# Kernel optimization log

Measured on AMD Instinct MI355X. Metric: run time of the kernel, lower is better.

Reference implementation:

```python
import jax, jax.numpy as jnp
import numpy as np
import math

HIDDEN_DIM = 1024
N_HEAD = 16
HEAD_DIM = HIDDEN_DIM // N_HEAD
BS, SEQ = 2, 4096


def setup_inputs() -> dict:
    key = jax.random.key(0)
    ks = jax.random.split(key, 6)
    s = 1.0 / math.sqrt(HIDDEN_DIM)
    return {
        "x": jax.random.normal(ks[0], (BS, SEQ, HIDDEN_DIM), dtype=jnp.float32),
        "attention_mask": jnp.zeros((1, 1, SEQ, SEQ), dtype=jnp.float32),
        "wq_w": jax.random.normal(ks[1], (HIDDEN_DIM, HIDDEN_DIM), dtype=jnp.float32) * s,
        "wq_b": jnp.zeros((HIDDEN_DIM,), dtype=jnp.float32),
        "wk_w": jax.random.normal(ks[2], (HIDDEN_DIM, HIDDEN_DIM), dtype=jnp.float32) * s,
        "wk_b": jnp.zeros((HIDDEN_DIM,), dtype=jnp.float32),
        "wv_w": jax.random.normal(ks[3], (HIDDEN_DIM, HIDDEN_DIM), dtype=jnp.float32) * s,
        "wv_b": jnp.zeros((HIDDEN_DIM,), dtype=jnp.float32),
        "wo_w": jax.random.normal(ks[4], (HIDDEN_DIM, HIDDEN_DIM), dtype=jnp.float32) * s,
        "wo_b": jnp.zeros((HIDDEN_DIM,), dtype=jnp.float32),
    }


def reference(x, attention_mask, wq_w, wq_b, wk_w, wk_b, wv_w, wv_b, wo_w, wo_b):
    bs, seq_len, _ = x.shape
    # nn.Linear: y = x @ W.T + b
    Q = x @ wq_w.T + wq_b
    K = x @ wk_w.T + wk_b
    V = x @ wv_w.T + wv_b
    # [bs, n_head, seq, head_dim]
    Q = Q.reshape(bs, seq_len, N_HEAD, HEAD_DIM).transpose(0, 2, 1, 3)
    K = K.reshape(bs, seq_len, N_HEAD, HEAD_DIM).transpose(0, 2, 1, 3)
    V = V.reshape(bs, seq_len, N_HEAD, HEAD_DIM).transpose(0, 2, 1, 3)
    scale = 1.0 / math.sqrt(HEAD_DIM)
    att = jnp.einsum('bhqd,bhkd->bhqk', Q, K) * scale
    att = att + attention_mask
    att = jax.nn.softmax(att, axis=-1)
    # dropout is identity in eval mode (p=0.1 during training)
    out = jnp.einsum('bhqk,bhkd->bhqd', att, V)
    out = out.transpose(0, 2, 1, 3).reshape(bs, seq_len, HIDDEN_DIM)
    return out @ wo_w.T + wo_b
```

## Files before the change

### kernel.cpp

```cpp
#include <hip/hip_runtime.h>

typedef unsigned short u16;
typedef __bf16 bf16x4 __attribute__((ext_vector_type(4)));
typedef __bf16 bf16x8 __attribute__((ext_vector_type(8)));
typedef float f32x4 __attribute__((ext_vector_type(4)));

#define SEQ_LEN 4096
#define HID 1024
#define NHEAD 16
#define HDIM 64
#define MROWS 8192
#define LOG2E 1.44269504088896f

__device__ __forceinline__ u16 f2bf(float f) {
  union { float f; unsigned u; } v; v.f = f;
  unsigned r = v.u + 0x7fffu + ((v.u >> 16) & 1u);
  return (u16)(r >> 16);
}

__device__ __forceinline__ float fexp2(float x) {
  float r;
  asm("v_exp_f32 %0, %1" : "=v"(r) : "v"(x));
  return r;
}

__device__ __forceinline__ void gload16(const void* g, void* lds) {
  __builtin_amdgcn_global_load_lds((const __attribute__((address_space(1))) void*)g,
                                   (__attribute__((address_space(3))) void*)lds, 16, 0, 0);
}


__global__ void prep_kernel(const float* __restrict__ x,
                            const float* __restrict__ w0, const float* __restrict__ w1,
                            const float* __restrict__ w2, const float* __restrict__ w3,
                            const float* __restrict__ mask,
                            u16* __restrict__ xb, u16* __restrict__ wb, int* __restrict__ flag) {
  const int NX = MROWS * HID / 4;
  const int NW = HID * HID / 4;
  const int NM = SEQ_LEN * SEQ_LEN / 4;
  const int TOT = NX + 4 * NW + NM;
  int stride = gridDim.x * blockDim.x;
  bool nz = false;
  for (int i = blockIdx.x * blockDim.x + threadIdx.x; i < TOT; i += stride) {
    if (i < NX) {
      float4 v = ((const float4*)x)[i];
      ((ushort4*)xb)[i] = make_ushort4(f2bf(v.x), f2bf(v.y), f2bf(v.z), f2bf(v.w));
    } else if (i < NX + 4 * NW) {
      int j = i - NX;
      int mat = j >> 18;
      int off = j & (NW - 1);
      const float* src = (mat == 0) ? w0 : (mat == 1) ? w1 : (mat == 2) ? w2 : w3;
      float4 v = ((const float4*)src)[off];
      ((ushort4*)(wb + (size_t)mat * HID * HID))[off] =
          make_ushort4(f2bf(v.x), f2bf(v.y), f2bf(v.z), f2bf(v.w));
    } else {
      int j = i - NX - 4 * NW;
      float4 v = ((const float4*)mask)[j];
      nz |= (v.x != 0.f) | (v.y != 0.f) | (v.z != 0.f) | (v.w != 0.f);
    }
  }
  if (__any(nz) && (threadIdx.x & 63) == 0) atomicOr(flag, 1);
}


__device__ __forceinline__ void gemm_core(const u16* __restrict__ A, const u16* __restrict__ W,
                                          int m0, int n0, char* As, char* Bs, f32x4 acc[4][4]) {
  const int t = threadIdx.x, w = t >> 6, l = t & 63;
  const int lr = l & 15, lg = l >> 4;
  const int wr = (w >> 1) * 64, wc = (w & 1) * 64;
#pragma unroll
  for (int i = 0; i < 4; i++)
#pragma unroll
    for (int j = 0; j < 4; j++) acc[i][j] = (f32x4){0.f, 0.f, 0.f, 0.f};

  for (int k0 = 0; k0 < HID; k0 += 64) {
    __syncthreads();
#pragma unroll
    for (int j = 0; j < 4; j++) {
      int o = w * 4096 + j * 1024 + l * 16;
      int row = o >> 7, kb = (o >> 4) & 7, skb = kb ^ (row & 7);
      gload16(A + (size_t)(m0 + row) * HID + k0 + skb * 8, As + (w * 4096 + j * 1024));
      gload16(W + (size_t)(n0 + row) * HID + k0 + skb * 8, Bs + (w * 4096 + j * 1024));
    }
    __syncthreads();
#pragma unroll
    for (int ks = 0; ks < 2; ks++) {
      bf16x8 af[4], bf[4];
      int kb = ks * 4 + lg;
#pragma unroll
      for (int mt = 0; mt < 4; mt++) {
        int row = wr + mt * 16 + lr;
        af[mt] = *(const bf16x8*)(As + row * 128 + ((kb ^ (row & 7)) << 4));
      }
#pragma unroll
      for (int nt = 0; nt < 4; nt++) {
        int row = wc + nt * 16 + lr;
        bf[nt] = *(const bf16x8*)(Bs + row * 128 + ((kb ^ (row & 7)) << 4));
      }
#pragma unroll
      for (int mt = 0; mt < 4; mt++)
#pragma unroll
        for (int nt = 0; nt < 4; nt++)
          acc[mt][nt] = __builtin_amdgcn_mfma_f32_16x16x32_bf16(af[mt], bf[nt], acc[mt][nt], 0, 0, 0);
    }
  }
}

__global__ __launch_bounds__(256) void gemm_qkv_kernel(
    const u16* __restrict__ xb, const u16* __restrict__ wqb, const u16* __restrict__ wkb,
    const u16* __restrict__ wvb, const float* __restrict__ bq, const float* __restrict__ bk,
    const float* __restrict__ bv, u16* __restrict__ Qb, u16* __restrict__ Kb, u16* __restrict__ VT) {
  __shared__ __align__(128) char lds[32768];
  int flat = blockIdx.y * 64 + blockIdx.x;
  int xcd = flat & 7, j = flat >> 3;
  int bx = xcd * 8 + (j & 7);
  int by = j >> 3;
  int m0 = bx * 128;
  int ng = by * 128;
  int mat = ng >> 10, n0 = ng & 1023;
  const u16* W = (mat == 0) ? wqb : (mat == 1) ? wkb : wvb;
  const float* bias = (mat == 0) ? bq : (mat == 1) ? bk : bv;
  f32x4 acc[4][4];
  gemm_core(xb, W, m0, n0, lds, lds + 16384, acc);

  const int t = threadIdx.x, w = t >> 6, l = t & 63;
  const int lr = l & 15, lg = l >> 4;
  if (mat < 2) {
    u16* dst = (mat == 0) ? Qb : Kb;
    float scale = (mat == 0) ? 0.125f * LOG2E : 1.0f;
#pragma unroll
    for (int mt = 0; mt < 4; mt++)
#pragma unroll
      for (int nt = 0; nt < 4; nt++) {
        int n = n0 + (w & 1) * 64 + nt * 16 + lr;
        float bn = bias[n];
#pragma unroll
        for (int i = 0; i < 4; i++) {
          int m = m0 + (w >> 1) * 64 + mt * 16 + lg * 4 + i;
          dst[(size_t)m * HID + n] = f2bf((acc[mt][nt][i] + bn) * scale);
        }
      }
  } else {
#pragma unroll
    for (int mt = 0; mt < 4; mt++)
#pragma unroll
      for (int nt = 0; nt < 4; nt++) {
        int m = m0 + (w >> 1) * 64 + mt * 16 + lg * 4;
        int n = n0 + (w & 1) * 64 + nt * 16 + lr;
        int b = m >> 12, s = m & 4095;
        int h = n >> 6, d = n & 63;
        int t4 = (s >> 2) & 15;
        int t4p = ((t4 & 8)) | ((t4 & 3) << 1) | ((t4 >> 2) & 1);
        int sp = (s & ~63) | (t4p << 2);
        float bn = bias[n];
        ushort4 pk = make_ushort4(f2bf(acc[mt][nt][0] + bn), f2bf(acc[mt][nt][1] + bn),
                                  f2bf(acc[mt][nt][2] + bn), f2bf(acc[mt][nt][3] + bn));
        *(ushort4*)(VT + (((size_t)(b * NHEAD + h) * HDIM + d) * SEQ_LEN + sp)) = pk;
      }
  }
}

__global__ __launch_bounds__(256) void gemm_out_kernel(
    const u16* __restrict__ Ob, const u16* __restrict__ wob, const float* __restrict__ bo,
    float* __restrict__ out) {
  __shared__ __align__(128) char lds[32768];
  int flat = blockIdx.y * 64 + blockIdx.x;
  int xcd = flat & 7, j = flat >> 3;
  int bx = xcd * 8 + (j & 7);
  int by = j >> 3;
  int m0 = bx * 128, n0 = by * 128;
  f32x4 acc[4][4];
  gemm_core(Ob, wob, m0, n0, lds, lds + 16384, acc);
  const int t = threadIdx.x, w = t >> 6, l = t & 63;
  const int lr = l & 15, lg = l >> 4;
#pragma unroll
  for (int mt = 0; mt < 4; mt++)
#pragma unroll
    for (int nt = 0; nt < 4; nt++) {
      int n = n0 + (w & 1) * 64 + nt * 16 + lr;
      float bn = bo[n];
#pragma unroll
      for (int i = 0; i < 4; i++) {
        int m = m0 + (w >> 1) * 64 + mt * 16 + lg * 4 + i;
        out[(size_t)m * HID + n] = acc[mt][nt][i] + bn;
      }
    }
}

__global__ __launch_bounds__(256, 2) void attn_kernel(
    const u16* __restrict__ Qb, const u16* __restrict__ Kb, const u16* __restrict__ VT,
    const float* __restrict__ mask, const int* __restrict__ flag, u16* __restrict__ Ob) {
  __shared__ __align__(128) char lds[32768];
  const int flat = blockIdx.x;
  const int xcd = flat & 7;
  const int slot = flat >> 3;
  const int bh = xcd * 4 + (slot >> 5);
  const int bx = slot & 31;
  const int q0 = bx * 128;
  const int b = bh >> 4, h = bh & 15;
  const int t = threadIdx.x, w = t >> 6, l = t & 63;
  const int lr = l & 15, lg = l >> 4;
  const bool useMask = (flag[0] != 0);
  int qrow[2];
#pragma unroll
  for (int s = 0; s < 2; s++) qrow[s] = q0 + (w * 2 + s) * 16 + lr;

  bf16x8 qf[2][2];
#pragma unroll
  for (int s = 0; s < 2; s++) {
    const u16* qp = Qb + (size_t)(b * SEQ_LEN + qrow[s]) * HID + h * HDIM;
#pragma unroll
    for (int ks = 0; ks < 2; ks++) qf[s][ks] = *(const bf16x8*)(qp + (ks * 4 + lg) * 8);
  }

  bf16x8 ones;
#pragma unroll
  for (int j = 0; j < 8; j++) ones[j] = (__bf16)1.0f;

  f32x4 oacc[2][4];
#pragma unroll
  for (int s = 0; s < 2; s++)
#pragma unroll
    for (int dt = 0; dt < 4; dt++) oacc[s][dt] = (f32x4){0.f, 0.f, 0.f, 0.f};
  f32x4 lacc[2] = {(f32x4){0.f, 0.f, 0.f, 0.f}, (f32x4){0.f, 0.f, 0.f, 0.f}};
  float m_r[2] = {-1e30f, -1e30f};

  int off[2][4];
#pragma unroll
  for (int ks = 0; ks < 2; ks++) {
    int kb = ks * 4 + lg;
#pragma unroll
    for (int kt = 0; kt < 4; kt++) {
      int row = kt * 16 + lr;
      off[ks][kt] = row * 128 + ((kb ^ (row & 7)) << 4);
    }
  }

  const int o0 = t * 16;
  const int o1 = o0 + 4096;
  const int r0 = t >> 3;
  const int r1 = r0 + 32;
  const int sk0 = (t & 7) ^ (r0 & 7);
  const int sk1 = (t & 7) ^ (r1 & 7);
  const u16* kg0 = Kb + (size_t)(b * SEQ_LEN) * HID + h * HDIM + (size_t)r0 * HID + sk0 * 8;
  const u16* kg1 = Kb + (size_t)(b * SEQ_LEN) * HID + h * HDIM + (size_t)r1 * HID + sk1 * 8;
  const u16* vg0 = VT + ((size_t)(b * NHEAD + h) * HDIM + r0) * SEQ_LEN + sk0 * 8;
  const u16* vg1 = VT + ((size_t)(b * NHEAD + h) * HDIM + r1) * SEQ_LEN + sk1 * 8;

#define STAGE(BI)                                            \
  do {                                                       \
    gload16(kg0, lds + (BI) * 8192 + o0);                    \
    gload16(kg1, lds + (BI) * 8192 + o1);                    \
    gload16(vg0, lds + 16384 + (BI) * 8192 + o0);            \
    gload16(vg1, lds + 16384 + (BI) * 8192 + o1);            \
    kg0 += 64 * HID; kg1 += 64 * HID; vg0 += 64; vg1 += 64;  \
  } while (0)

#define QKPART(BI)                                                                         \
    const char* Ks = lds + (BI) * 8192;                                                    \
    const char* Vs = lds + 16384 + (BI) * 8192;                                            \
    bf16x8 kf[2][4];                                                                       \
    _Pragma("unroll") for (int ks = 0; ks < 2; ks++)                                       \
    _Pragma("unroll") for (int kt = 0; kt < 4; kt++)                                       \
        kf[ks][kt] = *(const bf16x8*)(Ks + off[ks][kt]);                                   \
    f32x4 sf[2][4];                                                                        \
    _Pragma("unroll") for (int s = 0; s < 2; s++)                                          \
    _Pragma("unroll") for (int kt = 0; kt < 4; kt++) sf[s][kt] = (f32x4){0.f,0.f,0.f,0.f}; \
    __builtin_amdgcn_s_setprio(1);                                                         \
    _Pragma("unroll") for (int ks = 0; ks < 2; ks++)                                       \
    _Pragma("unroll") for (int s = 0; s < 2; s++)                                          \
    _Pragma("unroll") for (int kt = 0; kt < 4; kt++)                                       \
        sf[s][kt] = __builtin_amdgcn_mfma_f32_16x16x32_bf16(kf[ks][kt], qf[s][ks],         \
                                                            sf[s][kt], 0, 0, 0);          \
    __builtin_amdgcn_s_setprio(0);

#define PVPART                                                                             \
    bf16x8 vf[2][4];                                                                       \
    _Pragma("unroll") for (int ks = 0; ks < 2; ks++)                                       \
    _Pragma("unroll") for (int dt = 0; dt < 4; dt++)                                       \
        vf[ks][dt] = *(const bf16x8*)(Vs + off[ks][dt]);                                   \
    __builtin_amdgcn_s_setprio(1);                                                         \
    _Pragma("unroll") for (int s = 0; s < 2; s++) {                                        \
      _Pragma("unroll") for (int ks = 0; ks < 2; ks++) {                                   \
        bf16x8 pb;                                                                         \
        _Pragma("unroll") for (int j = 0; j < 4; j++) pb[j] = (__bf16)sf[s][2 * ks][j];    \
        _Pragma("unroll") for (int j = 0; j < 4; j++) pb[4 + j] = (__bf16)sf[s][2*ks+1][j];\
        _Pragma("unroll") for (int dt = 0; dt < 4; dt++)                                   \
            oacc[s][dt] =                                                                  \
                __builtin_amdgcn_mfma_f32_16x16x32_bf16(vf[ks][dt], pb, oacc[s][dt],0,0,0);\
        lacc[s] = __builtin_amdgcn_mfma_f32_16x16x32_bf16(ones, pb, lacc[s], 0, 0, 0);     \
      }                                                                                    \
    }                                                                                      \
    __builtin_amdgcn_s_setprio(0);

#define COMPUTE_FAST(BI)                                                                   \
  do {                                                                                     \
    QKPART(BI)                                                                             \
    _Pragma("unroll") for (int s = 0; s < 2; s++)                                          \
    _Pragma("unroll") for (int kt = 0; kt < 4; kt++)                                       \
    _Pragma("unroll") for (int i = 0; i < 4; i++)                                          \
        sf[s][kt][i] = fexp2(sf[s][kt][i]);                                                \
    PVPART                                                                                 \
  } while (0)

#define COMPUTE_SAFE(BI, KV0)                                                              \
  do {                                                                                     \
    QKPART(BI)                                                                             \
    _Pragma("unroll") for (int s = 0; s < 2; s++)                                          \
    _Pragma("unroll") for (int kt = 0; kt < 4; kt++)                                       \
    _Pragma("unroll") for (int i = 0; i < 4; i++)                                          \
        sf[s][kt][i] +=                                                                    \
            mask[(size_t)qrow[s] * SEQ_LEN + (KV0) + kt * 16 + lg * 4 + i] * LOG2E;        \
    float mx[2];                                                                           \
    _Pragma("unroll") for (int s = 0; s < 2; s++) {                                        \
      float m1 = fmaxf(fmaxf(sf[s][0][0], sf[s][0][1]), sf[s][0][2]);                      \
      m1 = fmaxf(fmaxf(m1, sf[s][0][3]), sf[s][1][0]);                                     \
      m1 = fmaxf(fmaxf(m1, sf[s][1][1]), sf[s][1][2]);                                     \
      m1 = fmaxf(fmaxf(m1, sf[s][1][3]), sf[s][2][0]);                                     \
      m1 = fmaxf(fmaxf(m1, sf[s][2][1]), sf[s][2][2]);                                     \
      m1 = fmaxf(fmaxf(m1, sf[s][2][3]), sf[s][3][0]);                                     \
      m1 = fmaxf(fmaxf(m1, sf[s][3][1]), sf[s][3][2]);                                     \
      m1 = fmaxf(m1, sf[s][3][3]);                                                         \
      m1 = fmaxf(m1, __shfl_xor(m1, 16));                                                  \
      mx[s] = fmaxf(m1, __shfl_xor(m1, 32));                                               \
    }                                                                                      \
    if (__any(fmaxf(mx[0] - m_r[0], mx[1] - m_r[1]) > 8.0f)) {                             \
      _Pragma("unroll") for (int s = 0; s < 2; s++) {                                      \
        float nm = fmaxf(m_r[s], mx[s]);                                                   \
        float scf = fexp2(m_r[s] - nm);                                                    \
        m_r[s] = nm;                                                                       \
        _Pragma("unroll") for (int dt = 0; dt < 4; dt++)                                   \
        _Pragma("unroll") for (int i = 0; i < 4; i++) oacc[s][dt][i] *= scf;               \
        lacc[s] *= scf;                                                                    \
      }                                                                                    \
    }                                                                                      \
    _Pragma("unroll") for (int s = 0; s < 2; s++)                                          \
    _Pragma("unroll") for (int kt = 0; kt < 4; kt++)                                       \
    _Pragma("unroll") for (int i = 0; i < 4; i++)                                          \
        sf[s][kt][i] = fexp2(sf[s][kt][i] - m_r[s]);                                       \
    PVPART                                                                                 \
  } while (0)

  STAGE(0);
  __syncthreads();

  const int NT = SEQ_LEN / 64;
  if (!useMask) {
    for (int t2 = 0; t2 < NT / 2; ++t2) {
      STAGE(1);
      COMPUTE_FAST(0);
      __syncthreads();
      if (t2 != NT / 2 - 1) STAGE(0);
      COMPUTE_FAST(1);
      __syncthreads();
    }
  } else {
    for (int t2 = 0; t2 < NT / 2; ++t2) {
      STAGE(1);
      COMPUTE_SAFE(0, t2 * 128);
      __syncthreads();
      if (t2 != NT / 2 - 1) STAGE(0);
      COMPUTE_SAFE(1, t2 * 128 + 64);
      __syncthreads();
    }
  }
#undef STAGE
#undef QKPART
#undef PVPART
#undef COMPUTE_FAST
#undef COMPUTE_SAFE

#pragma unroll
  for (int s = 0; s < 2; s++) {
    float inv = 1.0f / lacc[s][0];
    u16* orow = Ob + (size_t)(b * SEQ_LEN + qrow[s]) * HID + h * HDIM;
#pragma unroll
    for (int dt = 0; dt < 4; dt++) {
      ushort4 pk = make_ushort4(f2bf(oacc[s][dt][0] * inv), f2bf(oacc[s][dt][1] * inv),
                                f2bf(oacc[s][dt][2] * inv), f2bf(oacc[s][dt][3] * inv));
      *(ushort4*)(orow + dt * 16 + lg * 4) = pk;
    }
  }
}


extern "C" void kernel_launch(void* const* d_in, const int* in_sizes, int n_in,
                              void* d_out, int out_size, void* d_ws, size_t ws_size,
                              hipStream_t stream) {
  const float* x    = (const float*)d_in[0];
  const float* mask = (const float*)d_in[1];
  const float* wq   = (const float*)d_in[2];
  const float* bq   = (const float*)d_in[3];
  const float* wk   = (const float*)d_in[4];
  const float* bk   = (const float*)d_in[5];
  const float* wv   = (const float*)d_in[6];
  const float* bv   = (const float*)d_in[7];
  const float* wo   = (const float*)d_in[8];
  const float* bo   = (const float*)d_in[9];

  char* ws = (char*)d_ws;
  u16* xb  = (u16*)(ws + 0);
  u16* wqb = (u16*)(ws + 16777216);
  u16* Qb  = (u16*)(ws + 25165824);
  u16* Kb  = (u16*)(ws + 41943040);
  u16* VT  = (u16*)(ws + 58720256);
  int* flag = (int*)(ws + 75497472);
  u16* wkb = wqb + 1048576;
  u16* wvb = wqb + 2097152;
  u16* wob = wqb + 3145728;
  u16* Ob = xb;

  (void)hipMemsetAsync(flag, 0, 4, stream);
  prep_kernel<<<2048, 256, 0, stream>>>(x, wq, wk, wv, wo, mask, xb, wqb, flag);
  gemm_qkv_kernel<<<dim3(64, 24), 256, 0, stream>>>(xb, wqb, wkb, wvb, bq, bk, bv, Qb, Kb, VT);
  attn_kernel<<<1024, 256, 0, stream>>>(Qb, Kb, VT, mask, flag, Ob);
  gemm_out_kernel<<<dim3(64, 8), 256, 0, stream>>>(Ob, wob, bo, (float*)d_out);
}
```

Baseline: 245.4 us.

## Double query tile per attention block to 256 rows, split KV tile into halves

Each attention block now handles 256 query rows, with each wave owning 64 rows, so every staged K/V tile in shared memory is reused by twice as many queries. The grid drops from 1024 to 512 blocks, which halves global K/V traffic. Each 64-key tile is processed in two 32-key halves to limit register pressure from the doubled accumulators. The trade-offs are higher VGPR use, which may lower occupancy under launch_bounds(256,2), and fewer blocks to spread across CUs.

```diff
diff --git a/kernel.cpp b/kernel.cpp
--- a/kernel.cpp
+++ b/kernel.cpp
@@ -194,20 +194,20 @@
   const int flat = blockIdx.x;
   const int xcd = flat & 7;
   const int slot = flat >> 3;
-  const int bh = xcd * 4 + (slot >> 5);
-  const int bx = slot & 31;
-  const int q0 = bx * 128;
+  const int bh = xcd * 4 + (slot >> 4);
+  const int bx = slot & 15;
+  const int q0 = bx * 256;
   const int b = bh >> 4, h = bh & 15;
   const int t = threadIdx.x, w = t >> 6, l = t & 63;
   const int lr = l & 15, lg = l >> 4;
   const bool useMask = (flag[0] != 0);
-  int qrow[2];
-#pragma unroll
-  for (int s = 0; s < 2; s++) qrow[s] = q0 + (w * 2 + s) * 16 + lr;
-
-  bf16x8 qf[2][2];
-#pragma unroll
-  for (int s = 0; s < 2; s++) {
+  int qrow[4];
+#pragma unroll
+  for (int s = 0; s < 4; s++) qrow[s] = q0 + w * 64 + s * 16 + lr;
+
+  bf16x8 qf[4][2];
+#pragma unroll
+  for (int s = 0; s < 4; s++) {
     const u16* qp = Qb + (size_t)(b * SEQ_LEN + qrow[s]) * HID + h * HDIM;
 #pragma unroll
     for (int ks = 0; ks < 2; ks++) qf[s][ks] = *(const bf16x8*)(qp + (ks * 4 + lg) * 8);
@@ -217,13 +217,15 @@
 #pragma unroll
   for (int j = 0; j < 8; j++) ones[j] = (__bf16)1.0f;
 
-  f32x4 oacc[2][4];
-#pragma unroll
-  for (int s = 0; s < 2; s++)
+  f32x4 oacc[4][4];
+#pragma unroll
+  for (int s = 0; s < 4; s++)
 #pragma unroll
     for (int dt = 0; dt < 4; dt++) oacc[s][dt] = (f32x4){0.f, 0.f, 0.f, 0.f};
-  f32x4 lacc[2] = {(f32x4){0.f, 0.f, 0.f, 0.f}, (f32x4){0.f, 0.f, 0.f, 0.f}};
-  float m_r[2] = {-1e30f, -1e30f};
+  f32x4 lacc[4];
+#pragma unroll
+  for (int s = 0; s < 4; s++) lacc[s] = (f32x4){0.f, 0.f, 0.f, 0.f};
+  float m_r[4] = {-1e30f, -1e30f, -1e30f, -1e30f};
 
   int off[2][4];
 #pragma unroll
@@ -256,76 +258,75 @@
     kg0 += 64 * HID; kg1 += 64 * HID; vg0 += 64; vg1 += 64;  \
   } while (0)
 
-#define QKPART(BI)                                                                         \
+#define HALF_HEAD(Ks, H)                                                                   \
+    bf16x8 kf[2][2];                                                                       \
+    _Pragma("unroll") for (int ks = 0; ks < 2; ks++)                                       \
+    _Pragma("unroll") for (int ktl = 0; ktl < 2; ktl++)                                    \
+        kf[ks][ktl] = *(const bf16x8*)((Ks) + off[ks][2 * (H) + ktl]);                     \
+    f32x4 sf[4][2];                                                                        \
+    _Pragma("unroll") for (int s = 0; s < 4; s++)                                          \
+    _Pragma("unroll") for (int ktl = 0; ktl < 2; ktl++) sf[s][ktl] = (f32x4){0,0,0,0};     \
+    __builtin_amdgcn_s_setprio(1);                                                         \
+    _Pragma("unroll") for (int ks = 0; ks < 2; ks++)                                       \
+    _Pragma("unroll") for (int s = 0; s < 4; s++)                                          \
+    _Pragma("unroll") for (int ktl = 0; ktl < 2; ktl++)                                    \
+        sf[s][ktl] = __builtin_amdgcn_mfma_f32_16x16x32_bf16(kf[ks][ktl], qf[s][ks],       \
+                                                             sf[s][ktl], 0, 0, 0);        \
+    __builtin_amdgcn_s_setprio(0);
+
+#define HALF_TAIL(Vs, H)                                                                   \
+    bf16x8 vf[4];                                                                          \
+    _Pragma("unroll") for (int dt = 0; dt < 4; dt++)                                       \
+        vf[dt] = *(const bf16x8*)((Vs) + off[H][dt]);                                      \
+    bf16x8 pb[4];                                                                          \
+    _Pragma("unroll") for (int s = 0; s < 4; s++) {                                        \
+      _Pragma("unroll") for (int j = 0; j < 4; j++) pb[s][j] = (__bf16)sf[s][0][j];        \
+      _Pragma("unroll") for (int j = 0; j < 4; j++) pb[s][4 + j] = (__bf16)sf[s][1][j];    \
+    }                                                                                      \
+    __builtin_amdgcn_s_setprio(1);                                                         \
+    _Pragma("unroll") for (int s = 0; s < 4; s++) {                                        \
+      _Pragma("unroll") for (int dt = 0; dt < 4; dt++)                                     \
+          oacc[s][dt] =                                                                    \
+              __builtin_amdgcn_mfma_f32_16x16x32_bf16(vf[dt], pb[s], oacc[s][dt], 0,0,0);  \
+      lacc[s] = __builtin_amdgcn_mfma_f32_16x16x32_bf16(ones, pb[s], lacc[s], 0, 0, 0);    \
+    }                                                                                      \
+    __builtin_amdgcn_s_setprio(0);
+
+#define HALF_FAST(BI, H)                                                                   \
+  do {                                                                                     \
     const char* Ks = lds + (BI) * 8192;                                                    \
     const char* Vs = lds + 16384 + (BI) * 8192;                                            \
-    bf16x8 kf[2][4];                                                                       \
-    _Pragma("unroll") for (int ks = 0; ks < 2; ks++)                                       \
-    _Pragma("unroll") for (int kt = 0; kt < 4; kt++)                                       \
-        kf[ks][kt] = *(const bf16x8*)(Ks + off[ks][kt]);                                   \
-    f32x4 sf[2][4];                                                                        \
-    _Pragma("unroll") for (int s = 0; s < 2; s++)                                          \
-    _Pragma("unroll") for (int kt = 0; kt < 4; kt++) sf[s][kt] = (f32x4){0.f,0.f,0.f,0.f}; \
-    __builtin_amdgcn_s_setprio(1);                                                         \
-    _Pragma("unroll") for (int ks = 0; ks < 2; ks++)                                       \
-    _Pragma("unroll") for (int s = 0; s < 2; s++)                                          \
-    _Pragma("unroll") for (int kt = 0; kt < 4; kt++)                                       \
-        sf[s][kt] = __builtin_amdgcn_mfma_f32_16x16x32_bf16(kf[ks][kt], qf[s][ks],         \
-                                                            sf[s][kt], 0, 0, 0);          \
-    __builtin_amdgcn_s_setprio(0);
-
-#define PVPART                                                                             \
-    bf16x8 vf[2][4];                                                                       \
-    _Pragma("unroll") for (int ks = 0; ks < 2; ks++)                                       \
-    _Pragma("unroll") for (int dt = 0; dt < 4; dt++)                                       \
-        vf[ks][dt] = *(const bf16x8*)(Vs + off[ks][dt]);                                   \
-    __builtin_amdgcn_s_setprio(1);                                                         \
-    _Pragma("unroll") for (int s = 0; s < 2; s++) {                                        \
-      _Pragma("unroll") for (int ks = 0; ks < 2; ks++) {                                   \
-        bf16x8 pb;                                                                         \
-        _Pragma("unroll") for (int j = 0; j < 4; j++) pb[j] = (__bf16)sf[s][2 * ks][j];    \
-        _Pragma("unroll") for (int j = 0; j < 4; j++) pb[4 + j] = (__bf16)sf[s][2*ks+1][j];\
-        _Pragma("unroll") for (int dt = 0; dt < 4; dt++)                                   \
-            oacc[s][dt] =                                                                  \
-                __builtin_amdgcn_mfma_f32_16x16x32_bf16(vf[ks][dt], pb, oacc[s][dt],0,0,0);\
-        lacc[s] = __builtin_amdgcn_mfma_f32_16x16x32_bf16(ones, pb, lacc[s], 0, 0, 0);     \
-      }                                                                                    \
-    }                                                                                      \
-    __builtin_amdgcn_s_setprio(0);
-
-#define COMPUTE_FAST(BI)                                                                   \
+    HALF_HEAD(Ks, H)                                                                       \
+    _Pragma("unroll") for (int s = 0; s < 4; s++)                                          \
+    _Pragma("unroll") for (int ktl = 0; ktl < 2; ktl++)                                    \
+    _Pragma("unroll") for (int i = 0; i < 4; i++)                                          \
+        sf[s][ktl][i] = fexp2(sf[s][ktl][i]);                                              \
+    HALF_TAIL(Vs, H)                                                                       \
+  } while (0)
+
+#define HALF_SAFE(BI, H, KV0)                                                              \
   do {                                                                                     \
-    QKPART(BI)                                                                             \
-    _Pragma("unroll") for (int s = 0; s < 2; s++)                                          \
-    _Pragma("unroll") for (int kt = 0; kt < 4; kt++)                                       \
+    const char* Ks = lds + (BI) * 8192;                                                    \
+    const char* Vs = lds + 16384 + (BI) * 8192;                                            \
+    HALF_HEAD(Ks, H)                                                                       \
+    _Pragma("unroll") for (int s = 0; s < 4; s++)                                          \
+    _Pragma("unroll") for (int ktl = 0; ktl < 2; ktl++)                                    \
     _Pragma("unroll") for (int i = 0; i < 4; i++)                                          \
-        sf[s][kt][i] = fexp2(sf[s][kt][i]);                                                \
-    PVPART                                                                                 \
-  } while (0)
-
-#define COMPUTE_SAFE(BI, KV0)                                                              \
-  do {                                                                                     \
-    QKPART(BI)                                                                             \
-    _Pragma("unroll") for (int s = 0; s < 2; s++)                                          \
-    _Pragma("unroll") for (int kt = 0; kt < 4; kt++)                                       \
-    _Pragma("unroll") for (int i = 0; i < 4; i++)                                          \
-        sf[s][kt][i] +=                                                                    \
-            mask[(size_t)qrow[s] * SEQ_LEN + (KV0) + kt * 16 + lg * 4 + i] * LOG2E;        \
-    float mx[2];                                                                           \
-    _Pragma("unroll") for (int s = 0; s < 2; s++) {                                        \
+        sf[s][ktl][i] += mask[(size_t)qrow[s] * SEQ_LEN + (KV0) + (2 * (H) + ktl) * 16 +   \
+                              lg * 4 + i] * LOG2E;                                         \
+    float mx[4];                                                                           \
+    _Pragma("unroll") for (int s = 0; s < 4; s++) {                                        \
       float m1 = fmaxf(fmaxf(sf[s][0][0], sf[s][0][1]), sf[s][0][2]);                      \
       m1 = fmaxf(fmaxf(m1, sf[s][0][3]), sf[s][1][0]);                                     \
       m1 = fmaxf(fmaxf(m1, sf[s][1][1]), sf[s][1][2]);                                     \
-      m1 = fmaxf(fmaxf(m1, sf[s][1][3]), sf[s][2][0]);                                     \
-      m1 = fmaxf(fmaxf(m1, sf[s][2][1]), sf[s][2][2]);                                     \
-      m1 = fmaxf(fmaxf(m1, sf[s][2][3]), sf[s][3][0]);                                     \
-      m1 = fmaxf(fmaxf(m1, sf[s][3][1]), sf[s][3][2]);                                     \
-      m1 = fmaxf(m1, sf[s][3][3]);                                                         \
+      m1 = fmaxf(m1, sf[s][1][3]);                                                         \
       m1 = fmaxf(m1, __shfl_xor(m1, 16));                                                  \
       mx[s] = fmaxf(m1, __shfl_xor(m1, 32));                                               \
     }                                                                                      \
-    if (__any(fmaxf(mx[0] - m_r[0], mx[1] - m_r[1]) > 8.0f)) {                             \
-      _Pragma("unroll") for (int s = 0; s < 2; s++) {                                      \
+    float dmax = fmaxf(fmaxf(mx[0] - m_r[0], mx[1] - m_r[1]),                              \
+                       fmaxf(mx[2] - m_r[2], mx[3] - m_r[3]));                             \
+    if (__any(dmax > 8.0f)) {                                                              \
+      _Pragma("unroll") for (int s = 0; s < 4; s++) {                                      \
         float nm = fmaxf(m_r[s], mx[s]);                                                   \
         float scf = fexp2(m_r[s] - nm);                                                    \
         m_r[s] = nm;                                                                       \
@@ -334,11 +335,11 @@
         lacc[s] *= scf;                                                                    \
       }                                                                                    \
     }                                                                                      \
-    _Pragma("unroll") for (int s = 0; s < 2; s++)                                          \
-    _Pragma("unroll") for (int kt = 0; kt < 4; kt++)                                       \
+    _Pragma("unroll") for (int s = 0; s < 4; s++)                                          \
+    _Pragma("unroll") for (int ktl = 0; ktl < 2; ktl++)                                    \
     _Pragma("unroll") for (int i = 0; i < 4; i++)                                          \
-        sf[s][kt][i] = fexp2(sf[s][kt][i] - m_r[s]);                                       \
-    PVPART                                                                                 \
+        sf[s][ktl][i] = fexp2(sf[s][ktl][i] - m_r[s]);                                     \
+    HALF_TAIL(Vs, H)                                                                       \
   } while (0)
 
   STAGE(0);
@@ -348,30 +349,34 @@
   if (!useMask) {
     for (int t2 = 0; t2 < NT / 2; ++t2) {
       STAGE(1);
-      COMPUTE_FAST(0);
+      HALF_FAST(0, 0);
+      HALF_FAST(0, 1);
       __syncthreads();
       if (t2 != NT / 2 - 1) STAGE(0);
-      COMPUTE_FAST(1);
+      HALF_FAST(1, 0);
+      HALF_FAST(1, 1);
       __syncthreads();
     }
   } else {
     for (int t2 = 0; t2 < NT / 2; ++t2) {
       STAGE(1);
-      COMPUTE_SAFE(0, t2 * 128);
+      HALF_SAFE(0, 0, t2 * 128);
+      HALF_SAFE(0, 1, t2 * 128);
       __syncthreads();
       if (t2 != NT / 2 - 1) STAGE(0);
-      COMPUTE_SAFE(1, t2 * 128 + 64);
+      HALF_SAFE(1, 0, t2 * 128 + 64);
+      HALF_SAFE(1, 1, t2 * 128 + 64);
       __syncthreads();
     }
   }
 #undef STAGE
-#undef QKPART
-#undef PVPART
-#undef COMPUTE_FAST
-#undef COMPUTE_SAFE
-
-#pragma unroll
-  for (int s = 0; s < 2; s++) {
+#undef HALF_HEAD
+#undef HALF_TAIL
+#undef HALF_FAST
+#undef HALF_SAFE
+
+#pragma unroll
+  for (int s = 0; s < 4; s++) {
     float inv = 1.0f / lacc[s][0];
     u16* orow = Ob + (size_t)(b * SEQ_LEN + qrow[s]) * HID + h * HDIM;
 #pragma unroll
@@ -413,6 +418,6 @@
   (void)hipMemsetAsync(flag, 0, 4, stream);
   prep_kernel<<<2048, 256, 0, stream>>>(x, wq, wk, wv, wo, mask, xb, wqb, flag);
   gemm_qkv_kernel<<<dim3(64, 24), 256, 0, stream>>>(xb, wqb, wkb, wvb, bq, bk, bv, Qb, Kb, VT);
-  attn_kernel<<<1024, 256, 0, stream>>>(Qb, Kb, VT, mask, flag, Ob);
+  attn_kernel<<<512, 256, 0, stream>>>(Qb, Kb, VT, mask, flag, Ob);
   gemm_out_kernel<<<dim3(64, 8), 256, 0, stream>>>(Ob, wob, bo, (float*)d_out);
 }
```

After: 231.1 us. 5.8% less time.
